# Kernel optimization log

Hardware: AMD Instinct MI355X
Metric: run time of the kernel (lower is better)

Reference implementation:

```python
import jax, jax.numpy as jnp
import numpy as np

B, S, D = 8, 512, 768
HEADS = 16           # label_n
HD = 64              # size_per_head
NEG = 1e12


def setup_inputs() -> dict:
    key = jax.random.key(0)
    k1, k2, k3 = jax.random.split(key, 3)
    hidden = jax.random.normal(k1, (B, S, D), dtype=jnp.float32)
    token_ids = jax.random.randint(k2, (B, S), 0, 21128, dtype=jnp.int32)
    W = jax.random.normal(k3, (D, HEADS * 2 * HD), dtype=jnp.float32) * 0.02
    b = jnp.zeros((HEADS * 2 * HD,), dtype=jnp.float32)
    return {"hidden": hidden, "token_ids": token_ids, "W": W, "b": b}


def _rope(x):
    # x: [B, S, H, HD] -> RoPE-rotated, Su Jianlin interleaved convention
    d = x.shape[-1]
    inv_freq = 1.0 / (10000.0 ** (jnp.arange(0, d, 2, dtype=jnp.float32) / d))  # [d/2]
    pos = jnp.arange(x.shape[1], dtype=jnp.float32)                              # [S]
    freqs = pos[:, None] * inv_freq[None, :]                                     # [S, d/2]
    sin = jnp.repeat(jnp.sin(freqs), 2, axis=-1)[None, :, None, :]               # [1,S,1,d]
    cos = jnp.repeat(jnp.cos(freqs), 2, axis=-1)[None, :, None, :]
    x2 = jnp.stack([-x[..., 1::2], x[..., 0::2]], axis=-1).reshape(x.shape)
    return x * cos + x2 * sin


def reference(hidden, token_ids, W, b):
    # qk projection: [B,S,H,2,HD]
    qk = (hidden @ W + b).reshape(B, S, HEADS, 2, HD)
    q, k = qk[..., 0, :], qk[..., 1, :]          # [B,S,H,HD]
    q = _rope(q)
    k = _rope(k)
    # all-pairs span scores per entity head
    logits = jnp.einsum('bmhd,bnhd->bhmn', q, k) / jnp.sqrt(jnp.float32(HD))
    # padding mask from token ids (0 = pad)
    mask = (token_ids > 0).astype(logits.dtype)  # [B,S]
    logits = logits - (1.0 - mask[:, None, :, None]) * NEG
    logits = logits - (1.0 - mask[:, None, None, :]) * NEG
    # strict lower-triangular mask (spans must have start <= end)
    tril = jnp.tril(jnp.ones((S, S), dtype=logits.dtype), k=-1)
    logits = logits - tril[None, None, :, :] * NEG
    # valid-span weight mask (upper triangle incl. diag, both positions valid)
    tri_mask = (1.0 - tril)[None, None, :, :] * mask[:, None, :, None] * mask[:, None, None, :]
    return logits, tri_mask
```

## Files before the change

kernel.cpp:

```cpp
#include <hip/hip_runtime.h>
#include <hip/hip_bf16.h>
#include <cstdint>
#include <cstddef>


#define NEGV 1.0e12f

typedef short bf16x8 __attribute__((ext_vector_type(8)));
typedef float f32x4  __attribute__((ext_vector_type(4)));

static __device__ __forceinline__ short f2b(float x) {
    __hip_bfloat16 h = __float2bfloat16(x);
    union { __hip_bfloat16 h; short s; } u; u.h = h; return u.s;
}
static __device__ __forceinline__ float b2f(short s) {
    union { short s; __hip_bfloat16 h; } u; u.s = s; return __bfloat162float(u.h);
}
static __device__ __forceinline__ void gload16(const short* g, short* l) {
    __builtin_amdgcn_global_load_lds(
        (const __attribute__((address_space(1))) void*)g,
        (__attribute__((address_space(3))) void*)l, 16, 0, 0);
}

__global__ __launch_bounds__(256) void prep_kernel(const float* __restrict__ hidden,
                                                   const float* __restrict__ W,
                                                   short* __restrict__ Xb,
                                                   short* __restrict__ Wt,
                                                   float* __restrict__ SinT,
                                                   float* __restrict__ CosT) {
    __shared__ short T[64 * 68];
    int blk = blockIdx.x, tid = threadIdx.x;
    if (blk < 1536) {
        int t = blk * 256 + tid;
        const float4* hp = (const float4*)hidden;
        float4 a = hp[t * 2], c = hp[t * 2 + 1];
        bf16x8 v;
        v[0] = f2b(a.x); v[1] = f2b(a.y); v[2] = f2b(a.z); v[3] = f2b(a.w);
        v[4] = f2b(c.x); v[5] = f2b(c.y); v[6] = f2b(c.z); v[7] = f2b(c.w);
        *(bf16x8*)(Xb + t * 8) = v;
    } else if (blk < 1600) {
        int u = (blk - 1536) * 256 + tid;
        int s = u >> 5, i = u & 31;
        float ang = (float)s * exp2f(-0.4152410118609203f * (float)i);
        float sn, cs; __sincosf(ang, &sn, &cs);
        SinT[u] = sn; CosT[u] = cs;
    } else {
        int tb = blk - 1600;
        int k0 = (tb % 12) * 64, n0 = (tb / 12) * 64;
        int r = tid >> 2, cb = (tid & 3) * 4;
#pragma unroll
        for (int q = 0; q < 4; ++q) {
            int c = cb + q * 16;
            float4 v = *(const float4*)(W + (size_t)(k0 + r) * 2048 + n0 + c);
            short* tp = T + r * 68 + c;
            tp[0] = f2b(v.x); tp[1] = f2b(v.y); tp[2] = f2b(v.z); tp[3] = f2b(v.w);
        }
        __syncthreads();
        int n = tid >> 2, kc = (tid & 3) * 16;
        bf16x8 o0, o1;
#pragma unroll
        for (int j = 0; j < 8; ++j) {
            o0[j] = T[(kc + j) * 68 + n];
            o1[j] = T[(kc + 8 + j) * 68 + n];
        }
        short* wp = Wt + (size_t)(n0 + n) * 768 + k0 + kc;
        *(bf16x8*)wp = o0;
        *(bf16x8*)(wp + 8) = o1;
    }
}

__global__ __launch_bounds__(256) void gemm_rope(const short* __restrict__ A,
                                                 const short* __restrict__ Bt,
                                                 const float* __restrict__ bias,
                                                 const float* __restrict__ SinT,
                                                 const float* __restrict__ CosT,
                                                 short* __restrict__ Qb,
                                                 short* __restrict__ Kb) {
    __shared__ short As[128 * 64];
    __shared__ short Bs[128 * 64];
    const int blk = (blockIdx.x & 7) * 64 + (blockIdx.x >> 3);
    const int m0 = (blk >> 4) * 128;
    const int n0 = (blk & 15) * 128;
    const int tid  = threadIdx.x;
    const int wave = tid >> 6, lane = tid & 63;
    const int quad = lane >> 4, r16 = lane & 15;
    const int wm = (wave >> 1) * 64, wn = (wave & 1) * 64;

    const int sc  = ((lane & 7) ^ (lane >> 3)) * 8;
    const int rst = wave * 8 + (lane >> 3);
    const short* gA = A  + (size_t)(m0 + rst) * 768 + sc;
    const short* gB = Bt + (size_t)(n0 + rst) * 768 + sc;
    short* lA = As + (wave * 8) * 64;
    short* lB = Bs + (wave * 8) * 64;

    const int sw8 = r16 & 7;

    f32x4 acc[4][4] = {};
    for (int k0 = 0; k0 < 768; k0 += 64) {
        __syncthreads();
#pragma unroll
        for (int j = 0; j < 4; ++j) {
            gload16(gA + (size_t)j * 32 * 768 + k0, lA + j * 32 * 64);
            gload16(gB + (size_t)j * 32 * 768 + k0, lB + j * 32 * 64);
        }
        __syncthreads();

#pragma unroll
        for (int kk = 0; kk < 2; ++kk) {
            bf16x8 af[4], bfr[4];
#pragma unroll
            for (int mi = 0; mi < 4; ++mi)
                af[mi] = *(const bf16x8*)(As + (wm + mi * 16 + r16) * 64
                                             + ((kk * 4 + quad) ^ sw8) * 8);
#pragma unroll
            for (int ni = 0; ni < 4; ++ni)
                bfr[ni] = *(const bf16x8*)(Bs + (wn + ni * 16 + r16) * 64
                                              + ((kk * 4 + quad) ^ sw8) * 8);
#pragma unroll
            for (int mi = 0; mi < 4; ++mi)
#pragma unroll
                for (int ni = 0; ni < 4; ++ni)
                    acc[mi][ni] = __builtin_amdgcn_mfma_f32_16x16x32_bf16(
                        af[mi], bfr[ni], acc[mi][ni], 0, 0, 0);
        }
    }

    const int b     = m0 >> 9;
    const int s0l   = (m0 & 511) + wm + quad * 4;
    const int h     = n0 >> 7;
    const int which = wn >> 6;
    short* dstT = (which ? Kb : Qb) + (size_t)(b * 16 + h) * 512 * 64;
    const float sgn = (r16 & 1) ? 1.0f : -1.0f;
#pragma unroll
    for (int ni = 0; ni < 4; ++ni) {
        int col = n0 + wn + ni * 16 + r16;
        float bv = bias[col];
        int d  = ni * 16 + r16;
        int ii = d >> 1;
#pragma unroll
        for (int mi = 0; mi < 4; ++mi)
#pragma unroll
            for (int r = 0; r < 4; ++r) {
                int s = s0l + mi * 16 + r;
                float v  = acc[mi][ni][r] + bv;
                float pv = __shfl_xor(v, 1);
                float sn = SinT[s * 32 + ii];
                float cs = CosT[s * 32 + ii];
                dstT[(size_t)s * 64 + d] = f2b(v * cs + sgn * pv * sn);
            }
    }
}

__global__ __launch_bounds__(256) void logits_kernel(const short* __restrict__ Qb,
                                                     const short* __restrict__ Kb,
                                                     const int* __restrict__ tok,
                                                     float* __restrict__ out,
                                                     float* __restrict__ out2) {
    __shared__ short Qs[128 * 64];
    __shared__ short Ks[128 * 64];
    __shared__ float rowNeg[128];
    __shared__ float colNeg[128];

    int blk = (blockIdx.x & 7) * 256 + (blockIdx.x >> 3);
    int nt = blk & 3, mt = (blk >> 2) & 3, bh = blk >> 4;
    int b = bh >> 4, h = bh & 15;
    int m0 = mt * 128, n0 = nt * 128;

    const int tid  = threadIdx.x;
    const int wave = tid >> 6, lane = tid & 63;
    const int quad = lane >> 4, r16 = lane & 15;
    const int wm = (wave >> 1) * 64, wn = (wave & 1) * 64;

    if (mt > nt) {
        if (tid < 128)      rowNeg[tid]       = (tok[b * 512 + m0 + tid] > 0) ? 0.f : NEGV;
        else if (tid < 256) colNeg[tid - 128] = (tok[b * 512 + n0 + (tid - 128)] > 0) ? 0.f : NEGV;
        __syncthreads();
        float* obase = out + (size_t)bh * 512 * 512;
#pragma unroll
        for (int mi = 0; mi < 4; ++mi)
#pragma unroll
            for (int ni = 0; ni < 4; ++ni) {
                int n = n0 + wn + ni * 16 + r16;
                float cn = colNeg[n - n0];
#pragma unroll
                for (int r = 0; r < 4; ++r) {
                    int m = m0 + wm + mi * 16 + quad * 4 + r;
                    obase[(size_t)m * 512 + n] = -rowNeg[m - m0] - cn - NEGV;
                }
            }
        if (h == 0) {
            float* o2 = out2 + (size_t)b * 512 * 512;
#pragma unroll
            for (int mi = 0; mi < 4; ++mi)
#pragma unroll
                for (int ni = 0; ni < 4; ++ni) {
                    int n = n0 + wn + ni * 16 + r16;
#pragma unroll
                    for (int r = 0; r < 4; ++r) {
                        int m = m0 + wm + mi * 16 + quad * 4 + r;
                        o2[(size_t)m * 512 + n] = 0.f;
                    }
                }
        }
        return;
    }

    const short* gsrc = (wave < 2)
        ? Qb + ((size_t)bh * 512 + m0) * 64
        : Kb + ((size_t)bh * 512 + n0) * 64;
    short* ldst = (wave < 2) ? Qs : Ks;
    const int wv = wave & 1;
    const int gc = ((lane & 7) ^ (lane >> 3)) * 8;
    const int rl = wv * 64 + (lane >> 3);
#pragma unroll
    for (int j = 0; j < 8; ++j)
        gload16(gsrc + (rl + j * 8) * 64 + gc, ldst + wv * 4096 + j * 512);

    if (tid < 128)      rowNeg[tid]       = (tok[b * 512 + m0 + tid] > 0) ? 0.f : NEGV;
    else if (tid < 256) colNeg[tid - 128] = (tok[b * 512 + n0 + (tid - 128)] > 0) ? 0.f : NEGV;
    __syncthreads();

    const int sw8 = r16 & 7;
    f32x4 acc[4][4] = {};
#pragma unroll
    for (int kb = 0; kb < 2; ++kb) {
        bf16x8 af[4], bfr[4];
#pragma unroll
        for (int mi = 0; mi < 4; ++mi)
            af[mi] = *(const bf16x8*)(Qs + (wm + mi * 16 + r16) * 64
                                         + ((quad + kb * 4) ^ sw8) * 8);
#pragma unroll
        for (int ni = 0; ni < 4; ++ni)
            bfr[ni] = *(const bf16x8*)(Ks + (wn + ni * 16 + r16) * 64
                                          + ((quad + kb * 4) ^ sw8) * 8);
#pragma unroll
        for (int mi = 0; mi < 4; ++mi)
#pragma unroll
            for (int ni = 0; ni < 4; ++ni)
                acc[mi][ni] = __builtin_amdgcn_mfma_f32_16x16x32_bf16(
                    af[mi], bfr[ni], acc[mi][ni], 0, 0, 0);
    }

    float* obase = out + (size_t)bh * 512 * 512;
#pragma unroll
    for (int mi = 0; mi < 4; ++mi)
#pragma unroll
        for (int ni = 0; ni < 4; ++ni) {
            int n = n0 + wn + ni * 16 + r16;
            float cn = colNeg[n - n0];
#pragma unroll
            for (int r = 0; r < 4; ++r) {
                int m = m0 + wm + mi * 16 + quad * 4 + r;
                float v = acc[mi][ni][r] * 0.125f - rowNeg[m - m0] - cn
                          - ((m > n) ? NEGV : 0.0f);
                obase[(size_t)m * 512 + n] = v;
            }
        }

    if (h == 0) {
        float* o2 = out2 + (size_t)b * 512 * 512;
#pragma unroll
        for (int mi = 0; mi < 4; ++mi)
#pragma unroll
            for (int ni = 0; ni < 4; ++ni) {
                int n = n0 + wn + ni * 16 + r16;
                float mn = (colNeg[n - n0] == 0.f) ? 1.f : 0.f;
#pragma unroll
                for (int r = 0; r < 4; ++r) {
                    int m = m0 + wm + mi * 16 + quad * 4 + r;
                    float mm = (rowNeg[m - m0] == 0.f) ? 1.f : 0.f;
                    o2[(size_t)m * 512 + n] = (m > n) ? 0.f : (mm * mn);
                }
            }
    }
}

extern "C" void kernel_launch(void* const* d_in, const int* in_sizes, int n_in,
                              void* d_out, int out_size, void* d_ws, size_t ws_size,
                              hipStream_t stream) {
    const float* hidden = (const float*)d_in[0];
    const int*   tok    = (const int*)d_in[1];
    const float* W      = (const float*)d_in[2];
    const float* bias   = (const float*)d_in[3];
    float* out  = (float*)d_out;
    float* out2 = out + 33554432;

    char* ws = (char*)d_ws;
    short* Xb   = (short*)(ws);
    short* Wt   = (short*)(ws + 6291456);
    float* SinT = (float*)(ws + 9437184);
    float* CosT = (float*)(ws + 9502720);
    short* Qb   = (short*)(ws + 9568256);
    short* Kb   = (short*)(ws + 17956864);

    hipLaunchKernelGGL(prep_kernel,   dim3(1984), dim3(256), 0, stream,
                       hidden, W, Xb, Wt, SinT, CosT);
    hipLaunchKernelGGL(gemm_rope,     dim3(512),  dim3(256), 0, stream,
                       Xb, Wt, bias, SinT, CosT, Qb, Kb);
    hipLaunchKernelGGL(logits_kernel, dim3(2048), dim3(256), 0, stream,
                       Qb, Kb, tok, out, out2);
}
```

Baseline: 186.4 us.

## Double-buffer LDS tiles in the projection GEMM with async prefetch

Turns the single-buffered A/B shared-memory tiles in gemm_rope into two buffers and prefetches the k-tile two steps ahead with global_load_lds, using explicit vmcnt waits and raw s_barrier in place of two __syncthreads per iteration. The goal is to overlap global-to-LDS loads with MFMA compute in the GEMM main loop. In exchange it doubles LDS use (64KB per block), which may lower occupancy, and correctness now depends on the hand-counted vmcnt values. This is only the GEMM part of a multi-kernel pipeline whose large logits output write probably dominates total time.

```diff
diff --git a/kernel.cpp b/kernel.cpp
--- a/kernel.cpp
+++ b/kernel.cpp
@@ -76,8 +76,8 @@
                                                  const float* __restrict__ CosT,
                                                  short* __restrict__ Qb,
                                                  short* __restrict__ Kb) {
-    __shared__ short As[128 * 64];
-    __shared__ short Bs[128 * 64];
+    __shared__ short As[2][128 * 64];
+    __shared__ short Bs[2][128 * 64];
     const int blk = (blockIdx.x & 7) * 64 + (blockIdx.x >> 3);
     const int m0 = (blk >> 4) * 128;
     const int n0 = (blk & 15) * 128;
@@ -90,31 +90,42 @@
     const int rst = wave * 8 + (lane >> 3);
     const short* gA = A  + (size_t)(m0 + rst) * 768 + sc;
     const short* gB = Bt + (size_t)(n0 + rst) * 768 + sc;
-    short* lA = As + (wave * 8) * 64;
-    short* lB = Bs + (wave * 8) * 64;
+    const int lbase = (wave * 8) * 64;
 
     const int sw8 = r16 & 7;
 
     f32x4 acc[4][4] = {};
-    for (int k0 = 0; k0 < 768; k0 += 64) {
-        __syncthreads();
+
+    auto stage = [&](int t, int buf) {
+        const int k0 = t * 64;
 #pragma unroll
         for (int j = 0; j < 4; ++j) {
-            gload16(gA + (size_t)j * 32 * 768 + k0, lA + j * 32 * 64);
-            gload16(gB + (size_t)j * 32 * 768 + k0, lB + j * 32 * 64);
-        }
-        __syncthreads();
+            gload16(gA + (size_t)(j * 32) * 768 + k0, As[buf] + lbase + j * 32 * 64);
+            gload16(gB + (size_t)(j * 32) * 768 + k0, Bs[buf] + lbase + j * 32 * 64);
+        }
+    };
+
+    stage(0, 0);
+    stage(1, 1);
+
+#pragma unroll
+    for (int t = 0; t < 12; ++t) {
+        const int cur = t & 1;
+        if (t < 11) { asm volatile("s_waitcnt vmcnt(8)" ::: "memory"); }
+        else        { asm volatile("s_waitcnt vmcnt(0)" ::: "memory"); }
+        __builtin_amdgcn_sched_barrier(0);
+        __builtin_amdgcn_s_barrier();
 
 #pragma unroll
         for (int kk = 0; kk < 2; ++kk) {
             bf16x8 af[4], bfr[4];
 #pragma unroll
             for (int mi = 0; mi < 4; ++mi)
-                af[mi] = *(const bf16x8*)(As + (wm + mi * 16 + r16) * 64
+                af[mi] = *(const bf16x8*)(As[cur] + (wm + mi * 16 + r16) * 64
                                              + ((kk * 4 + quad) ^ sw8) * 8);
 #pragma unroll
             for (int ni = 0; ni < 4; ++ni)
-                bfr[ni] = *(const bf16x8*)(Bs + (wn + ni * 16 + r16) * 64
+                bfr[ni] = *(const bf16x8*)(Bs[cur] + (wn + ni * 16 + r16) * 64
                                               + ((kk * 4 + quad) ^ sw8) * 8);
 #pragma unroll
             for (int mi = 0; mi < 4; ++mi)
@@ -123,6 +134,9 @@
                     acc[mi][ni] = __builtin_amdgcn_mfma_f32_16x16x32_bf16(
                         af[mi], bfr[ni], acc[mi][ni], 0, 0, 0);
         }
+
+        __builtin_amdgcn_s_barrier();
+        if (t + 2 < 12) stage(t + 2, cur);
     }
 
     const int b     = m0 >> 9;
```

Result: no change. 183.7 us (median of 2 runs) (-1.4%).
